# Performance work log

Measured on AMD Instinct MI355X. Metric: run time of the kernel, lower is better.

The kernel has to match this reference:

```python
import jax, jax.numpy as jnp
import numpy as np

B, S, IN_DIM, OUT_DIM = 16, 1024, 1024, 1024
NEG_SLOPE = 0.01  # torch F.leaky_relu default


def setup_inputs() -> dict:
    key = jax.random.key(0)
    ks = jax.random.split(key, 10)
    sc_in = 1.0 / np.sqrt(IN_DIM)
    sc_out = 1.0 / np.sqrt(OUT_DIM)
    return {
        "xs": jax.random.normal(ks[0], (B, S, IN_DIM), dtype=jnp.float32),
        "mask": jax.random.randint(ks[1], (B, S), 0, 2, dtype=jnp.int32),
        "Wk": jax.random.uniform(ks[2], (OUT_DIM, IN_DIM), jnp.float32, -sc_in, sc_in),
        "bk": jax.random.uniform(ks[3], (OUT_DIM,), jnp.float32, -sc_in, sc_in),
        "Wq": jax.random.uniform(ks[4], (OUT_DIM, IN_DIM), jnp.float32, -sc_in, sc_in),
        "bq": jax.random.uniform(ks[5], (OUT_DIM,), jnp.float32, -sc_in, sc_in),
        "Wv": jax.random.uniform(ks[6], (OUT_DIM, IN_DIM), jnp.float32, -sc_in, sc_in),
        "bv": jax.random.uniform(ks[7], (OUT_DIM,), jnp.float32, -sc_in, sc_in),
        "Wlin": jax.random.uniform(ks[8], (OUT_DIM, OUT_DIM), jnp.float32, -sc_out, sc_out),
        "blin": jax.random.uniform(ks[9], (OUT_DIM,), jnp.float32, -sc_out, sc_out),
    }


def reference(xs, mask, Wk, bk, Wq, bq, Wv, bv, Wlin, blin):
    # projections: torch Linear is x @ W.T + b
    K = jnp.einsum('bsi,oi->bso', xs, Wk) + bk  # [B,S,D]
    Q = jnp.einsum('bsi,oi->bso', xs, Wq) + bq  # [B,S,D]
    V = jnp.einsum('bsi,oi->bso', xs, Wv) + bv  # [B,S,D]
    # qk[b,s,e] = sum_d K[b,s,d] * Q[b,e,d]
    qk = jnp.einsum('bsd,bed->bse', K, Q) / xs.shape[-1]
    # mask.repeat(1,S).view(B,S,S) => element [b,i,j] = mask[b,j] (column/key mask)
    qk = jnp.where(mask[:, None, :].astype(bool), qk, -jnp.inf)
    a = jax.nn.softmax(qk, axis=-1)  # [B,S,S]
    # faithful to einsum('bij,bik->bik'): sum a over last axis, scale V elementwise
    attn = jnp.sum(a, axis=-1, keepdims=True) * V  # [B,S,D]
    out = jnp.einsum('bsd,od->bso', attn, Wlin) + blin
    return jnp.where(out >= 0, out, NEG_SLOPE * out)
```

## Files before the change

### kernel.cpp

```cpp
#include <hip/hip_runtime.h>
#include <hip/hip_bf16.h>
#include <stdint.h>


#define M_TOT 16384
#define KDIM  1024
#define NDIM  1024
#define NKT   32

typedef __attribute__((ext_vector_type(8))) short bf16x8;
typedef __attribute__((ext_vector_type(4))) float f32x4;
typedef __attribute__((ext_vector_type(4))) unsigned short u16x4;
typedef __attribute__((ext_vector_type(8))) unsigned short u16x8;

static __device__ __forceinline__ unsigned short f2bf(float f) {
    union { float f; unsigned int u; } v; v.f = f;
    unsigned int u = v.u;
    return (unsigned short)((u + 0x7fffu + ((u >> 16) & 1u)) >> 16);
}

static __device__ __forceinline__ u16x8 pack8(float4 a, float4 b) {
    u16x8 p = { f2bf(a.x), f2bf(a.y), f2bf(a.z), f2bf(a.w),
                f2bf(b.x), f2bf(b.y), f2bf(b.z), f2bf(b.w) };
    return p;
}

static __device__ __forceinline__ void gload16(const void* g, void* l) {
    __builtin_amdgcn_global_load_lds(
        (__attribute__((address_space(1))) void*)(g),
        (__attribute__((address_space(3))) void*)(l), 16, 0, 0);
}

static __device__ __forceinline__ int swz128(int p) {
    return p ^ (((p >> 7) & 7) << 4);
}

__global__ __launch_bounds__(256) void prep0_kernel(
    const float* __restrict__ Wv, const float* __restrict__ Wlin,
    const float* __restrict__ bv, const float* __restrict__ blin,
    unsigned short* __restrict__ Wvt, unsigned short* __restrict__ Wlb,
    float* __restrict__ bcomb) {
    __shared__ float Tl[64 * 65];
    const int bid = blockIdx.x;
    const int t = threadIdx.x;

    if (bid < 256) {
        const int dt = bid >> 4;
        const int it = bid & 15;
        const int r = t >> 2;
        const int c0 = (t & 3) * 16;
        #pragma unroll
        for (int u = 0; u < 4; ++u) {
            float4 v = *(const float4*)&Wv[((size_t)(dt * 64 + r)) * NDIM + it * 64 + c0 + 4 * u];
            Tl[r * 65 + c0 + 4 * u + 0] = v.x;
            Tl[r * 65 + c0 + 4 * u + 1] = v.y;
            Tl[r * 65 + c0 + 4 * u + 2] = v.z;
            Tl[r * 65 + c0 + 4 * u + 3] = v.w;
        }
        __syncthreads();
        const int i = t >> 2;
        const int dq = (t & 3) * 16;
        float v[16];
        #pragma unroll
        for (int u = 0; u < 16; ++u) v[u] = Tl[(dq + u) * 65 + i];
        u16x8 p0 = { f2bf(v[0]), f2bf(v[1]), f2bf(v[2]), f2bf(v[3]),
                     f2bf(v[4]), f2bf(v[5]), f2bf(v[6]), f2bf(v[7]) };
        u16x8 p1 = { f2bf(v[8]), f2bf(v[9]), f2bf(v[10]), f2bf(v[11]),
                     f2bf(v[12]), f2bf(v[13]), f2bf(v[14]), f2bf(v[15]) };
        unsigned short* dst = &Wvt[((size_t)(it * 64 + i)) * KDIM + dt * 64 + dq];
        *(u16x8*)dst = p0;
        *(u16x8*)(dst + 8) = p1;
    } else if (bid < 512) {
        const size_t idx = (((size_t)(bid - 256)) * 256 + t) * 16;
        float4 a = *(const float4*)&Wlin[idx];
        float4 b = *(const float4*)&Wlin[idx + 4];
        float4 c = *(const float4*)&Wlin[idx + 8];
        float4 d = *(const float4*)&Wlin[idx + 12];
        *(u16x8*)&Wlb[idx] = pack8(a, b);
        *(u16x8*)&Wlb[idx + 8] = pack8(c, d);
    } else {
        const int wave = t >> 6, lane = t & 63;
        const int o = (bid - 512) * 4 + wave;
        float s = 0.f;
        for (int d = lane; d < KDIM; d += 64) s += Wlin[o * KDIM + d] * bv[d];
        #pragma unroll
        for (int off = 32; off > 0; off >>= 1) s += __shfl_down(s, off, 64);
        if (lane == 0) bcomb[o] = s + blin[o];
    }
}

__global__ __launch_bounds__(256) void wcomb_kernel(
    const unsigned short* __restrict__ Wlb, const unsigned short* __restrict__ Wvt,
    unsigned short* __restrict__ Wc) {
    __shared__ unsigned short As[64 * 32];
    __shared__ unsigned short Bs[64 * 32];
    const int t = threadIdx.x;
    const int ot = blockIdx.x >> 4;
    const int it = blockIdx.x & 15;
    const int w = t >> 6, l = t & 63;
    const int wr = (w >> 1) * 32, wc = (w & 1) * 32;
    const int lr = l & 15, lk = l >> 4;

    f32x4 acc[2][2] = {};

    const unsigned short* gA = &Wlb[((size_t)(ot * 64 + (t >> 2))) * KDIM + (t & 3) * 8];
    const unsigned short* gB = &Wvt[((size_t)(it * 64 + (t >> 2))) * KDIM + (t & 3) * 8];
    unsigned short* lA = &As[w * 512];
    unsigned short* lB = &Bs[w * 512];

    for (int kt = 0; kt < KDIM / 32; ++kt) {
        gload16(gA + kt * 32, lA);
        gload16(gB + kt * 32, lB);
        __syncthreads();
        bf16x8 af[2], bfr[2];
        #pragma unroll
        for (int fi = 0; fi < 2; ++fi)
            af[fi] = *(bf16x8*)&As[(wr + fi * 16 + lr) * 32 + lk * 8];
        #pragma unroll
        for (int fj = 0; fj < 2; ++fj)
            bfr[fj] = *(bf16x8*)&Bs[(wc + fj * 16 + lr) * 32 + lk * 8];
        #pragma unroll
        for (int fi = 0; fi < 2; ++fi)
            #pragma unroll
            for (int fj = 0; fj < 2; ++fj)
                acc[fi][fj] = __builtin_amdgcn_mfma_f32_16x16x32_bf16(
                    af[fi], bfr[fj], acc[fi][fj], 0, 0, 0);
        __syncthreads();
    }
    #pragma unroll
    for (int fi = 0; fi < 2; ++fi)
        #pragma unroll
        for (int fj = 0; fj < 2; ++fj)
            #pragma unroll
            for (int r = 0; r < 4; ++r) {
                const int o = ot * 64 + wr + fi * 16 + lk * 4 + r;
                const int i = it * 64 + wc + fj * 16 + lr;
                Wc[(size_t)o * KDIM + i] = f2bf(acc[fi][fj][r]);
            }
}

__global__ __launch_bounds__(256, 3) void main_fused(
    const float* __restrict__ xs, const unsigned short* __restrict__ Wc,
    const float* __restrict__ bcomb, float* __restrict__ out) {
    __shared__ __align__(16) char As[8192];
    __shared__ __align__(16) char Bs[16384];
    const int t = threadIdx.x;
    const int w = t >> 6, l = t & 63;
    const int wm = w >> 1, wn = w & 1;
    const int lr = l & 15, lk = l >> 4;

    const int swzb = ((blockIdx.x & 7) << 7) | (blockIdx.x >> 3);
    const int mt = swzb >> 3, nt = swzb & 7;

    int aoff[4], boff[4];
    #pragma unroll
    for (int fi = 0; fi < 4; ++fi) {
        const int r = wm * 64 + fi * 16 + lr;
        aoff[fi] = swz128(((r >> 1) << 7) | ((r & 1) << 6) | (lk << 4));
    }
    #pragma unroll
    for (int fj = 0; fj < 4; ++fj) {
        const int r = wn * 64 + fj * 16 + lr;
        boff[fj] = swz128(((r >> 1) << 7) | ((r & 1) << 6) | (lk << 4));
    }

    const float* gAq[2];
    #pragma unroll
    for (int c = 0; c < 2; ++c) {
        const int q = c * 4096 + t * 16;
        const int p = swz128(q);
        const int r = ((p >> 7) << 1) | ((p >> 6) & 1);
        gAq[c] = xs + ((size_t)(mt * 128 + r)) * KDIM + ((p & 63) >> 1);
    }
    const int ldsA0 = t * 16;
    const int ldsA1 = 4096 + t * 16;

    const char* gBq[2];
    #pragma unroll
    for (int c = 0; c < 2; ++c) {
        const int q = c * 4096 + w * 1024 + l * 16;
        const int p = swz128(q);
        const int r = ((p >> 7) << 1) | ((p >> 6) & 1);
        gBq[c] = (const char*)Wc + ((size_t)(nt * 128 + r)) * 2048 + (p & 63);
    }
    const int ldsBw0 = w * 1024;
    const int ldsBw1 = 4096 + w * 1024;

    f32x4 acc[4][4] = {};
    float4 avA[4];

    avA[0] = *(const float4*)(gAq[0]);
    avA[1] = *(const float4*)(gAq[0] + 4);
    avA[2] = *(const float4*)(gAq[1]);
    avA[3] = *(const float4*)(gAq[1] + 4);
    gload16(gBq[0], Bs + ldsBw0);
    gload16(gBq[1], Bs + ldsBw1);

    for (int kt = 0; kt < NKT; ++kt) {
        char* bhalf = Bs + ((kt & 1) << 12);
        char* bnext = Bs + (((kt & 1) ^ 1) << 12);

        *(u16x8*)(As + ldsA0) = pack8(avA[0], avA[1]);
        *(u16x8*)(As + ldsA1) = pack8(avA[2], avA[3]);
        asm volatile("s_waitcnt vmcnt(0) lgkmcnt(0)" ::: "memory");
        __builtin_amdgcn_s_barrier();

        bf16x8 bfr[4], af[4];
        #pragma unroll
        for (int fj = 0; fj < 4; ++fj)
            bfr[fj] = *(const bf16x8*)(bhalf + boff[fj]);
        #pragma unroll
        for (int fi = 0; fi < 4; ++fi)
            af[fi] = *(const bf16x8*)(As + aoff[fi]);

        if (kt < NKT - 1) {
            avA[0] = *(const float4*)(gAq[0] + (kt + 1) * 32);
            avA[1] = *(const float4*)(gAq[0] + (kt + 1) * 32 + 4);
            avA[2] = *(const float4*)(gAq[1] + (kt + 1) * 32);
            avA[3] = *(const float4*)(gAq[1] + (kt + 1) * 32 + 4);
            gload16(gBq[0] + (size_t)(kt + 1) * 64, bnext + ldsBw0);
            gload16(gBq[1] + (size_t)(kt + 1) * 64, bnext + ldsBw1);
        }

        __builtin_amdgcn_s_setprio(1);
        #pragma unroll
        for (int fi = 0; fi < 4; ++fi)
            #pragma unroll
            for (int fj = 0; fj < 4; ++fj)
                acc[fi][fj] = __builtin_amdgcn_mfma_f32_16x16x32_bf16(
                    af[fi], bfr[fj], acc[fi][fj], 0, 0, 0);
        __builtin_amdgcn_s_setprio(0);

        asm volatile("s_waitcnt lgkmcnt(0)" ::: "memory");
        __builtin_amdgcn_s_barrier();
    }

    #pragma unroll
    for (int fi = 0; fi < 4; ++fi)
        #pragma unroll
        for (int fj = 0; fj < 4; ++fj) {
            const int col = nt * 128 + wn * 64 + fj * 16 + lr;
            const float b = bcomb[col];
            #pragma unroll
            for (int r = 0; r < 4; ++r) {
                const int row = mt * 128 + wm * 64 + fi * 16 + lk * 4 + r;
                float v = acc[fi][fj][r] + b;
                out[(size_t)row * NDIM + col] = v >= 0.f ? v : 0.01f * v;
            }
        }
}

__global__ __launch_bounds__(256) void main_gemm_f32(
    const float* __restrict__ X, const unsigned short* __restrict__ Wc,
    const float* __restrict__ bcomb, float* __restrict__ out) {
    __shared__ unsigned short As[128 * 32];
    __shared__ unsigned short Bs[128 * 32];
    const int t = threadIdx.x;
    const int nt = blockIdx.x & 7;
    const int mt = blockIdx.x >> 3;
    const int w = t >> 6, l = t & 63;
    const int wr = (w >> 1) * 64, wcc = (w & 1) * 64;
    const int lr = l & 15, lk = l >> 4;

    f32x4 acc[4][4] = {};

    const int arow = t >> 3;
    const int akq = t & 7;
    const int brow = t >> 2;
    const int bc4 = t & 3;

    for (int kt = 0; kt < KDIM / 32; ++kt) {
        float4 av[4];
        #pragma unroll
        for (int j = 0; j < 4; ++j) {
            const int row = j * 32 + arow;
            av[j] = *(const float4*)&X[(mt * 128 + row) * KDIM + kt * 32 + akq * 4];
        }
        __syncthreads();
        #pragma unroll
        for (int j = 0; j < 4; ++j) {
            const int row = j * 32 + arow;
            u16x4 p = { f2bf(av[j].x), f2bf(av[j].y), f2bf(av[j].z), f2bf(av[j].w) };
            *(u16x4*)&As[row * 32 + akq * 4] = p;
        }
        #pragma unroll
        for (int j = 0; j < 2; ++j) {
            const int row = j * 64 + brow;
            const unsigned short* g = &Wc[(nt * 128 + row) * KDIM + kt * 32 + bc4 * 8];
            unsigned short* ldst = &Bs[(j * 256 + w * 64) * 8];
            gload16(g, ldst);
        }
        __syncthreads();
        bf16x8 af[4], bfr[4];
        #pragma unroll
        for (int fi = 0; fi < 4; ++fi)
            af[fi] = *(bf16x8*)&As[(wr + fi * 16 + lr) * 32 + lk * 8];
        #pragma unroll
        for (int fj = 0; fj < 4; ++fj)
            bfr[fj] = *(bf16x8*)&Bs[(wcc + fj * 16 + lr) * 32 + lk * 8];
        #pragma unroll
        for (int fi = 0; fi < 4; ++fi)
            #pragma unroll
            for (int fj = 0; fj < 4; ++fj)
                acc[fi][fj] = __builtin_amdgcn_mfma_f32_16x16x32_bf16(
                    af[fi], bfr[fj], acc[fi][fj], 0, 0, 0);
    }

    #pragma unroll
    for (int fi = 0; fi < 4; ++fi)
        #pragma unroll
        for (int fj = 0; fj < 4; ++fj) {
            const int col = nt * 128 + wcc + fj * 16 + lr;
            const float b = bcomb[col];
            #pragma unroll
            for (int r = 0; r < 4; ++r) {
                const int row = mt * 128 + wr + fi * 16 + lk * 4 + r;
                float v = acc[fi][fj][r] + b;
                out[row * NDIM + col] = v >= 0.f ? v : 0.01f * v;
            }
        }
}

extern "C" void kernel_launch(void* const* d_in, const int* in_sizes, int n_in,
                              void* d_out, int out_size, void* d_ws, size_t ws_size,
                              hipStream_t stream) {
    const float* xs   = (const float*)d_in[0];
    const float* Wv   = (const float*)d_in[6];
    const float* bv   = (const float*)d_in[7];
    const float* Wlin = (const float*)d_in[8];
    const float* blin = (const float*)d_in[9];

    unsigned short* Wc = (unsigned short*)d_ws;
    float* bcomb = (float*)((char*)d_ws + 2097152);
    float* out = (float*)d_out;

    unsigned short* Wvt = (unsigned short*)d_out;
    unsigned short* Wlb = (unsigned short*)((char*)d_out + 2097152);

    const size_t NEED = 2101248;
    hipLaunchKernelGGL(prep0_kernel, dim3(768), dim3(256), 0, stream,
                       Wv, Wlin, bv, blin, Wvt, Wlb, bcomb);
    hipLaunchKernelGGL(wcomb_kernel, dim3(256), dim3(256), 0, stream,
                       Wlb, Wvt, Wc);
    if (ws_size >= NEED) {
        hipLaunchKernelGGL(main_fused, dim3((M_TOT / 128) * (NDIM / 128)),
                           dim3(256), 0, stream, xs, Wc, bcomb, out);
    } else {
        hipLaunchKernelGGL(main_gemm_f32, dim3((M_TOT / 128) * (NDIM / 128)),
                           dim3(256), 0, stream, xs, Wc, bcomb, out);
    }
}
```

Measured before the change: 83.19 us.

## Pre-convert xs to bf16 and use 256x128 tiles with async LDS loads

Adds a pass in the prep kernel that converts xs from fp32 to bf16 into workspace. The main GEMM now loads both A and B directly into LDS with global_load_lds and double buffers 24KB stages. Blocks grow to 512 threads covering 256x128 output tiles, which halves the grid and raises reuse of each B tile. The aim is to remove the register round-trip and in-loop fp32-to-bf16 packing from the GEMM. The cost is an extra read of xs plus a write and re-read of the bf16 copy, and more workspace.

```diff
diff --git a/kernel.cpp b/kernel.cpp
--- a/kernel.cpp
+++ b/kernel.cpp
@@ -35,14 +35,27 @@
     return p ^ (((p >> 7) & 7) << 4);
 }
 
-__global__ __launch_bounds__(256) void prep0_kernel(
+__global__ __launch_bounds__(256) void prep0x_kernel(
     const float* __restrict__ Wv, const float* __restrict__ Wlin,
     const float* __restrict__ bv, const float* __restrict__ blin,
-    unsigned short* __restrict__ Wvt, unsigned short* __restrict__ Wlb,
-    float* __restrict__ bcomb) {
+    const float* __restrict__ xs, unsigned short* __restrict__ Wvt,
+    unsigned short* __restrict__ Wlb, float* __restrict__ bcomb,
+    unsigned short* __restrict__ Xb) {
     __shared__ float Tl[64 * 65];
     const int bid = blockIdx.x;
     const int t = threadIdx.x;
+
+    if (bid >= 768) {
+        const size_t base = (((size_t)(bid - 768)) * 256 + t) * 8;
+        #pragma unroll
+        for (int itr = 0; itr < 4; ++itr) {
+            const size_t idx = base + (size_t)itr * (size_t)(2048 * 256 * 8);
+            float4 a = *(const float4*)&xs[idx];
+            float4 b = *(const float4*)&xs[idx + 4];
+            *(u16x8*)&Xb[idx] = pack8(a, b);
+        }
+        return;
+    }
 
     if (bid < 256) {
         const int dt = bid >> 4;
@@ -139,17 +152,16 @@
             }
 }
 
-__global__ __launch_bounds__(256, 3) void main_fused(
-    const float* __restrict__ xs, const unsigned short* __restrict__ Wc,
+__global__ __launch_bounds__(512, 4) void main_mb(
+    const unsigned short* __restrict__ Xb, const unsigned short* __restrict__ Wc,
     const float* __restrict__ bcomb, float* __restrict__ out) {
-    __shared__ __align__(16) char As[8192];
-    __shared__ __align__(16) char Bs[16384];
-    const int t = threadIdx.x;
-    const int w = t >> 6, l = t & 63;
+    extern __shared__ char lds[];
+    const int tid = threadIdx.x;
+    const int w = tid >> 6, l = tid & 63;
     const int wm = w >> 1, wn = w & 1;
     const int lr = l & 15, lk = l >> 4;
 
-    const int swzb = ((blockIdx.x & 7) << 7) | (blockIdx.x >> 3);
+    const int swzb = ((blockIdx.x & 7) << 6) | (blockIdx.x >> 3);
     const int mt = swzb >> 3, nt = swzb & 7;
 
     int aoff[4], boff[4];
@@ -161,66 +173,57 @@
     #pragma unroll
     for (int fj = 0; fj < 4; ++fj) {
         const int r = wn * 64 + fj * 16 + lr;
-        boff[fj] = swz128(((r >> 1) << 7) | ((r & 1) << 6) | (lk << 4));
-    }
-
-    const float* gAq[2];
+        boff[fj] = 16384 + swz128(((r >> 1) << 7) | ((r & 1) << 6) | (lk << 4));
+    }
+
+    const char* srcA[2];
     #pragma unroll
     for (int c = 0; c < 2; ++c) {
-        const int q = c * 4096 + t * 16;
+        const int q = c * 8192 + tid * 16;
         const int p = swz128(q);
         const int r = ((p >> 7) << 1) | ((p >> 6) & 1);
-        gAq[c] = xs + ((size_t)(mt * 128 + r)) * KDIM + ((p & 63) >> 1);
-    }
-    const int ldsA0 = t * 16;
-    const int ldsA1 = 4096 + t * 16;
-
-    const char* gBq[2];
-    #pragma unroll
-    for (int c = 0; c < 2; ++c) {
-        const int q = c * 4096 + w * 1024 + l * 16;
+        srcA[c] = (const char*)Xb + ((size_t)(mt * 256 + r)) * 2048 + (p & 63);
+    }
+    const char* srcB;
+    {
+        const int q = tid * 16;
         const int p = swz128(q);
         const int r = ((p >> 7) << 1) | ((p >> 6) & 1);
-        gBq[c] = (const char*)Wc + ((size_t)(nt * 128 + r)) * 2048 + (p & 63);
-    }
-    const int ldsBw0 = w * 1024;
-    const int ldsBw1 = 4096 + w * 1024;
+        srcB = (const char*)Wc + ((size_t)(nt * 128 + r)) * 2048 + (p & 63);
+    }
+    const int ldsAw = w * 1024;
+    const int ldsBw = 16384 + w * 1024;
 
     f32x4 acc[4][4] = {};
-    float4 avA[4];
-
-    avA[0] = *(const float4*)(gAq[0]);
-    avA[1] = *(const float4*)(gAq[0] + 4);
-    avA[2] = *(const float4*)(gAq[1]);
-    avA[3] = *(const float4*)(gAq[1] + 4);
-    gload16(gBq[0], Bs + ldsBw0);
-    gload16(gBq[1], Bs + ldsBw1);
+
+#define STAGE(TT, BUF)                                                         \
+    do {                                                                       \
+        gload16(srcA[0] + (size_t)(TT) * 64, (BUF) + ldsAw);                   \
+        gload16(srcA[1] + (size_t)(TT) * 64, (BUF) + 8192 + ldsAw);            \
+        gload16(srcB + (size_t)(TT) * 64, (BUF) + ldsBw);                      \
+    } while (0)
+
+    STAGE(0, lds);
 
     for (int kt = 0; kt < NKT; ++kt) {
-        char* bhalf = Bs + ((kt & 1) << 12);
-        char* bnext = Bs + (((kt & 1) ^ 1) << 12);
-
-        *(u16x8*)(As + ldsA0) = pack8(avA[0], avA[1]);
-        *(u16x8*)(As + ldsA1) = pack8(avA[2], avA[3]);
-        asm volatile("s_waitcnt vmcnt(0) lgkmcnt(0)" ::: "memory");
+        char* cbuf = lds + (kt & 1) * 24576;
+        char* nbuf = lds + ((kt & 1) ^ 1) * 24576;
+
+        if (kt < NKT - 1) {
+            STAGE(kt + 1, nbuf);
+            asm volatile("s_waitcnt vmcnt(3)" ::: "memory");
+        } else {
+            asm volatile("s_waitcnt vmcnt(0)" ::: "memory");
+        }
         __builtin_amdgcn_s_barrier();
 
-        bf16x8 bfr[4], af[4];
+        bf16x8 af[4], bfr[4];
+        #pragma unroll
+        for (int fi = 0; fi < 4; ++fi)
+            af[fi] = *(const bf16x8*)(cbuf + aoff[fi]);
         #pragma unroll
         for (int fj = 0; fj < 4; ++fj)
-            bfr[fj] = *(const bf16x8*)(bhalf + boff[fj]);
-        #pragma unroll
-        for (int fi = 0; fi < 4; ++fi)
-            af[fi] = *(const bf16x8*)(As + aoff[fi]);
-
-        if (kt < NKT - 1) {
-            avA[0] = *(const float4*)(gAq[0] + (kt + 1) * 32);
-            avA[1] = *(const float4*)(gAq[0] + (kt + 1) * 32 + 4);
-            avA[2] = *(const float4*)(gAq[1] + (kt + 1) * 32);
-            avA[3] = *(const float4*)(gAq[1] + (kt + 1) * 32 + 4);
-            gload16(gBq[0] + (size_t)(kt + 1) * 64, bnext + ldsBw0);
-            gload16(gBq[1] + (size_t)(kt + 1) * 64, bnext + ldsBw1);
-        }
+            bfr[fj] = *(const bf16x8*)(cbuf + boff[fj]);
 
         __builtin_amdgcn_s_setprio(1);
         #pragma unroll
@@ -231,9 +234,9 @@
                     af[fi], bfr[fj], acc[fi][fj], 0, 0, 0);
         __builtin_amdgcn_s_setprio(0);
 
-        asm volatile("s_waitcnt lgkmcnt(0)" ::: "memory");
         __builtin_amdgcn_s_barrier();
     }
+#undef STAGE
 
     #pragma unroll
     for (int fi = 0; fi < 4; ++fi)
@@ -243,7 +246,7 @@
             const float b = bcomb[col];
             #pragma unroll
             for (int r = 0; r < 4; ++r) {
-                const int row = mt * 128 + wm * 64 + fi * 16 + lk * 4 + r;
+                const int row = mt * 256 + wm * 64 + fi * 16 + lk * 4 + r;
                 float v = acc[fi][fj][r] + b;
                 out[(size_t)row * NDIM + col] = v >= 0.f ? v : 0.01f * v;
             }
@@ -332,20 +335,28 @@
 
     unsigned short* Wc = (unsigned short*)d_ws;
     float* bcomb = (float*)((char*)d_ws + 2097152);
+    unsigned short* Xb = (unsigned short*)((char*)d_ws + 2101248);
     float* out = (float*)d_out;
 
     unsigned short* Wvt = (unsigned short*)d_out;
     unsigned short* Wlb = (unsigned short*)((char*)d_out + 2097152);
 
-    const size_t NEED = 2101248;
-    hipLaunchKernelGGL(prep0_kernel, dim3(768), dim3(256), 0, stream,
-                       Wv, Wlin, bv, blin, Wvt, Wlb, bcomb);
-    hipLaunchKernelGGL(wcomb_kernel, dim3(256), dim3(256), 0, stream,
-                       Wlb, Wvt, Wc);
+    const size_t NEED = 2101248 + (size_t)M_TOT * KDIM * 2;
     if (ws_size >= NEED) {
-        hipLaunchKernelGGL(main_fused, dim3((M_TOT / 128) * (NDIM / 128)),
-                           dim3(256), 0, stream, xs, Wc, bcomb, out);
+        (void)hipFuncSetAttribute((const void*)main_mb,
+                                  hipFuncAttributeMaxDynamicSharedMemorySize,
+                                  49152);
+        hipLaunchKernelGGL(prep0x_kernel, dim3(768 + 2048), dim3(256), 0,
+                           stream, Wv, Wlin, bv, blin, xs, Wvt, Wlb, bcomb, Xb);
+        hipLaunchKernelGGL(wcomb_kernel, dim3(256), dim3(256), 0, stream,
+                           Wlb, Wvt, Wc);
+        hipLaunchKernelGGL(main_mb, dim3(512), dim3(512), 49152, stream,
+                           Xb, Wc, bcomb, out);
     } else {
+        hipLaunchKernelGGL(prep0x_kernel, dim3(768), dim3(256), 0, stream,
+                           Wv, Wlin, bv, blin, xs, Wvt, Wlb, bcomb, Xb);
+        hipLaunchKernelGGL(wcomb_kernel, dim3(256), dim3(256), 0, stream,
+                           Wlb, Wvt, Wc);
         hipLaunchKernelGGL(main_gemm_f32, dim3((M_TOT / 128) * (NDIM / 128)),
                            dim3(256), 0, stream, xs, Wc, bcomb, out);
     }
```

Result: faster. 75.31 us (-9.5%).
